# Kernel tuning notes

Measured on AMD Instinct MI355X. Metric: run time of the kernel, lower is better.

Reference implementation:

```python
import jax, jax.numpy as jnp
import numpy as np

H_MIN = -1.0
H_MAX = 1.0
B_SAT = 1.0
N = 256          # Preisach mesh size (n x n)
M = 4000         # number of applied-field time steps


def setup_inputs() -> dict:
    key = jax.random.key(0)
    k1, k2 = jax.random.split(key)
    # applied magnetic field history, spanning [h_min, h_max]
    h_data = jax.random.uniform(k1, (M,), dtype=jnp.float32, minval=-1.0, maxval=1.0)
    # raw (pre-softplus) hysteresis density vector, length n(n+1)/2
    raw = jax.random.normal(k2, (N * (N + 1) // 2,), dtype=jnp.float32)
    return {"h_data": h_data, "raw_hyst_density_vector": raw}


def reference(h_data, raw_hyst_density_vector):
    n = N
    dt = h_data.dtype
    x = jnp.linspace(0.0, 1.0, n, dtype=dt)
    # 'xy' indexing: xx varies along columns (beta thresholds), yy along rows (alpha thresholds)
    xx, yy = jnp.meshgrid(x, x)
    tril_mask = jnp.tril(jnp.ones((n, n), dtype=dt))

    # normalize_h
    h_norm = (h_data - H_MIN) / (H_MAX - H_MIN)
    hs = jnp.concatenate([jnp.full((1,), -H_MIN, dtype=dt), h_norm])  # (M+1,)
    # torch indexing hs[i-1] wraps to hs[-1] at i=0 -> roll by 1
    hp = jnp.roll(hs, 1)

    init = -jnp.ones((n, n), dtype=dt)

    def step(state, hh):
        h, p = hh
        swept_up = jnp.where(yy >= h, state, jnp.asarray(1.0, dt))    # sweep up: flip below alpha threshold
        swept_dn = jnp.where(xx <= h, state, jnp.asarray(-1.0, dt))   # sweep left: flip above beta threshold
        s = jnp.where(h > p, swept_up, jnp.where(h < p, swept_dn, state))
        s = s * tril_mask  # torch.tril each step
        return s, s

    _, states = jax.lax.scan(step, init, (hs, hp))  # (M+1, n, n)

    dens_vec = jax.nn.softplus(raw_hyst_density_vector)
    ti, tj = jnp.tril_indices(n)
    dens = jnp.zeros((n, n), dtype=dens_vec.dtype).at[ti, tj].set(dens_vec)
    a = B_SAT / jnp.sum(dens)

    # b[i] = sum(dens * states[i+1])
    b = jnp.einsum('tij,ij->t', states[1:], dens)
    return b * a
```

## Files before the change

### kernel.cpp

```cpp
#include <hip/hip_runtime.h>

#define NN 256
#define TT 32

__device__ __forceinline__ float softplus_f(float x) {
    if (x > 20.0f) return x;
    return log1pf(expf(x));
}

__global__ void __launch_bounds__(256)
kA(const float* __restrict__ h_g, const float* __restrict__ raw, int M, int G,
   float* __restrict__ PrefT, float* __restrict__ RowTot,
   int* __restrict__ steps_g, unsigned int* __restrict__ UDt)
{
    int b = blockIdx.x, tid = threadIdx.x;
    if (b < NN) {
        __shared__ float s[NN];
        float v = 0.0f;
        if (tid <= b) v = softplus_f(raw[b * (b + 1) / 2 + tid]);
        s[tid] = v;
        __syncthreads();
        for (int off = 1; off < NN; off <<= 1) {
            float add = (tid >= off) ? s[tid - off] : 0.0f;
            __syncthreads();
            s[tid] += add;
            __syncthreads();
        }
        PrefT[(tid + 1) * NN + b] = s[tid];
        if (tid == 0)      PrefT[b] = 0.0f;
        if (tid == NN - 1) RowTot[b] = s[tid];
    } else {
        __shared__ float xs[NN];
        __shared__ float hh[TT + 1];
        __shared__ int   dd[TT + 1];
        int c  = b - NN;
        int t0 = c * TT;
        int Tb = min(TT, M - t0);
        xs[tid] = (float)((double)tid / 255.0);
        __syncthreads();
        if (tid < Tb) {
            int tau = t0 + 1 + tid;
            float cur  = (h_g[tau - 1] + 1.0f) * 0.5f;
            float prev = (tau == 1) ? 1.0f : (h_g[tau - 2] + 1.0f) * 0.5f;
            int d = (cur > prev) ? 2 : ((cur < prev) ? 0 : 1);
            int lo = 0, hi = NN;
            while (lo < hi) { int m = (lo + hi) >> 1; if (xs[m] < cur) lo = m + 1; else hi = m; }
            int ih = lo;
            lo = 0; hi = NN;
            while (lo < hi) { int m = (lo + hi) >> 1; if (xs[m] <= cur) lo = m + 1; else hi = m; }
            int jh = lo;
            hh[1 + tid] = cur;
            dd[1 + tid] = d - 1;
            steps_g[tau] = d | (ih << 2) | (jh << 11);
        }
        __syncthreads();
        float xi = xs[tid];
        int Ue = 0, De = 0;
        for (int k = 1; k <= Tb; ++k) {
            float hv = hh[k]; int d = dd[k];
            if (d > 0 && hv > xi) Ue = t0 + k + 1;
            if (d < 0 && hv < xi) De = t0 + k + 1;
        }
        UDt[c * NN + tid] = (unsigned)Ue | ((unsigned)De << 16);
    }
}

__global__ void __launch_bounds__(256)
kB(const float* __restrict__ h_g, const int* __restrict__ steps_g,
   const unsigned int* __restrict__ UDt,
   const float* __restrict__ PrefT, const float* __restrict__ RowTot,
   float* __restrict__ out, int M)
{
    __shared__ int   rec_s[TT + 1];
    __shared__ int   Dv[NN];
    __shared__ float red[4 * (TT + 2)];
    __shared__ float tot[TT + 2];
    int b = blockIdx.x, tid = threadIdx.x;
    int t0 = b * TT;
    int Tb = min(TT, M - t0);

    if (tid < TT) rec_s[1 + tid] = (tid < Tb) ? steps_g[t0 + 1 + tid] : 0;
    float RT = RowTot[tid];

    float hsM = (h_g[M - 1] + 1.0f) * 0.5f;
    unsigned uM = (hsM < 1.0f && tid < NN - 1) ? 1u : 0u;
    unsigned dM = 0u;
    const unsigned int* p = UDt + tid;
    int k = 0;
    for (; k + 16 <= b; k += 16) {
        unsigned vv[16];
        #pragma unroll
        for (int u = 0; u < 16; ++u) vv[u] = p[(k + u) * NN];
        #pragma unroll
        for (int u = 0; u < 16; ++u) {
            unsigned ue = vv[u] & 0xFFFFu, de = vv[u] >> 16;
            if (ue > uM) uM = ue;
            if (de > dM) dM = de;
        }
    }
    for (; k < b; ++k) {
        unsigned v = p[k * NN];
        unsigned ue = v & 0xFFFFu, de = v >> 16;
        if (ue > uM) uM = ue;
        if (de > dM) dM = de;
    }
    int Ue = (int)uM;
    Dv[tid] = (int)dM;
    __syncthreads();

    float pk[TT + 1];
    #pragma unroll
    for (int kk = 1; kk <= TT; ++kk) {
        int jh = (rec_s[kk] >> 11) & 0x1FF;
        pk[kk] = PrefT[jh * NN + tid];
    }

    int lo = 0, hi = NN;
    while (lo < hi) { int m = (lo + hi) >> 1; if (Dv[m] < Ue) lo = m + 1; else hi = m; }
    int c = min(lo, tid + 1);
    float w = 2.0f * PrefT[c * NN + tid] - RT;

    float vals[TT + 2];
    vals[0] = RT; vals[1] = w;
    int cc = c; float ww = w;
    #pragma unroll
    for (int kk = 1; kk <= TT; ++kk) {
        float dl = 0.0f;
        if (kk <= Tb) {
            int rec = rec_s[kk];
            int d = rec & 3;
            if (d == 2) {
                int ih = (rec >> 2) & 0x1FF;
                if (tid < ih) { dl = RT - ww; ww = RT; cc = tid + 1; }
            } else if (d == 0) {
                int jh = (rec >> 11) & 0x1FF;
                if (cc > jh) { float wn = 2.0f * pk[kk] - RT; dl = wn - ww; ww = wn; cc = jh; }
            }
        }
        vals[1 + kk] = dl;
    }

    #pragma unroll
    for (int q = 0; q < TT + 2; ++q)
        for (int off = 32; off; off >>= 1)
            vals[q] += __shfl_down(vals[q], off, 64);
    int lane = tid & 63, wv = tid >> 6;
    if (lane == 0) {
        #pragma unroll
        for (int q = 0; q < TT + 2; ++q) red[wv * (TT + 2) + q] = vals[q];
    }
    __syncthreads();
    if (tid < TT + 2)
        tot[tid] = red[tid] + red[(TT + 2) + tid] + red[2 * (TT + 2) + tid] + red[3 * (TT + 2) + tid];
    __syncthreads();
    if (tid < TT) {
        float x = tot[2 + tid];
        #pragma unroll
        for (int off = 1; off < TT; off <<= 1) {
            float y = __shfl_up(x, off, 64);
            if (tid >= off) x += y;
        }
        if (tid < Tb) out[t0 + tid] = (tot[1] + x) * (1.0f / tot[0]);
    }
}

extern "C" void kernel_launch(void* const* d_in, const int* in_sizes, int n_in,
                              void* d_out, int out_size, void* d_ws, size_t ws_size,
                              hipStream_t stream) {
    const float* h   = (const float*)d_in[0];
    const float* raw = (const float*)d_in[1];
    float* out = (float*)d_out;
    int M = in_sizes[0];
    int G = (M + TT - 1) / TT;

    char* ws = (char*)d_ws;
    size_t off = 0;
    auto take = [&](size_t bytes) { size_t cur = off; off = (off + bytes + 255) & ~(size_t)255; return cur; };
    float*        PrefT  = (float*)(ws + take((size_t)(NN + 1) * NN * 4));
    float*        RowTot = (float*)(ws + take((size_t)NN * 4));
    int*          steps  = (int*)(ws + take((size_t)(M + 1) * 4));
    unsigned int* UDt    = (unsigned int*)(ws + take((size_t)G * NN * 4));

    kA<<<NN + G, 256, 0, stream>>>(h, raw, M, G, PrefT, RowTot, steps, UDt);
    kB<<<G, 256, 0, stream>>>(h, steps, UDt, PrefT, RowTot, out, M);
}
```

Before: 69.71 us.

## Fuse two-kernel Preisach pipeline into one kernel with per-block redundant recomputation

Merges the precompute kernel and the per-chunk evaluation kernel into a single launch. Each block rescans all prior time steps with atomicMax into shared buckets and suffix/prefix max scans, replacing the global UDt table. It also recomputes the softplus row prefix sums serially per thread, taking only the needed prefix values through a sorted request list in shared memory. This removes a launch and the global intermediates, but every block repeats O(M) step processing and O(N) softplus work per thread, about 125 blocks each doing redundant work.

```diff
diff --git a/kernel.cpp b/kernel.cpp
--- a/kernel.cpp
+++ b/kernel.cpp
@@ -9,120 +9,102 @@
 }
 
 __global__ void __launch_bounds__(256)
-kA(const float* __restrict__ h_g, const float* __restrict__ raw, int M, int G,
-   float* __restrict__ PrefT, float* __restrict__ RowTot,
-   int* __restrict__ steps_g, unsigned int* __restrict__ UDt)
+kFused(const float* __restrict__ h_g, const float* __restrict__ raw,
+       float* __restrict__ out, int M)
 {
-    int b = blockIdx.x, tid = threadIdx.x;
-    if (b < NN) {
-        __shared__ float s[NN];
-        float v = 0.0f;
-        if (tid <= b) v = softplus_f(raw[b * (b + 1) / 2 + tid]);
-        s[tid] = v;
-        __syncthreads();
-        for (int off = 1; off < NN; off <<= 1) {
-            float add = (tid >= off) ? s[tid - off] : 0.0f;
-            __syncthreads();
-            s[tid] += add;
-            __syncthreads();
-        }
-        PrefT[(tid + 1) * NN + b] = s[tid];
-        if (tid == 0)      PrefT[b] = 0.0f;
-        if (tid == NN - 1) RowTot[b] = s[tid];
-    } else {
-        __shared__ float xs[NN];
-        __shared__ float hh[TT + 1];
-        __shared__ int   dd[TT + 1];
-        int c  = b - NN;
-        int t0 = c * TT;
-        int Tb = min(TT, M - t0);
-        xs[tid] = (float)((double)tid / 255.0);
-        __syncthreads();
-        if (tid < Tb) {
-            int tau = t0 + 1 + tid;
-            float cur  = (h_g[tau - 1] + 1.0f) * 0.5f;
-            float prev = (tau == 1) ? 1.0f : (h_g[tau - 2] + 1.0f) * 0.5f;
-            int d = (cur > prev) ? 2 : ((cur < prev) ? 0 : 1);
-            int lo = 0, hi = NN;
-            while (lo < hi) { int m = (lo + hi) >> 1; if (xs[m] < cur) lo = m + 1; else hi = m; }
-            int ih = lo;
-            lo = 0; hi = NN;
-            while (lo < hi) { int m = (lo + hi) >> 1; if (xs[m] <= cur) lo = m + 1; else hi = m; }
-            int jh = lo;
-            hh[1 + tid] = cur;
-            dd[1 + tid] = d - 1;
-            steps_g[tau] = d | (ih << 2) | (jh << 11);
-        }
-        __syncthreads();
-        float xi = xs[tid];
-        int Ue = 0, De = 0;
-        for (int k = 1; k <= Tb; ++k) {
-            float hv = hh[k]; int d = dd[k];
-            if (d > 0 && hv > xi) Ue = t0 + k + 1;
-            if (d < 0 && hv < xi) De = t0 + k + 1;
-        }
-        UDt[c * NN + tid] = (unsigned)Ue | ((unsigned)De << 16);
-    }
-}
-
-__global__ void __launch_bounds__(256)
-kB(const float* __restrict__ h_g, const int* __restrict__ steps_g,
-   const unsigned int* __restrict__ UDt,
-   const float* __restrict__ PrefT, const float* __restrict__ RowTot,
-   float* __restrict__ out, int M)
-{
+    __shared__ float xs[NN];
+    __shared__ int   bestU[NN + 1];
+    __shared__ int   bestD[NN + 1];
     __shared__ int   rec_s[TT + 1];
-    __shared__ int   Dv[NN];
+    __shared__ int   plist[TT];
+    __shared__ float pk_s[TT][NN];
     __shared__ float red[4 * (TT + 2)];
     __shared__ float tot[TT + 2];
-    int b = blockIdx.x, tid = threadIdx.x;
-    int t0 = b * TT;
-    int Tb = min(TT, M - t0);
 
-    if (tid < TT) rec_s[1 + tid] = (tid < Tb) ? steps_g[t0 + 1 + tid] : 0;
-    float RT = RowTot[tid];
+    const int tid  = threadIdx.x;
+    const int c    = blockIdx.x;
+    const int t0   = c * TT;
+    const int Tb   = min(TT, M - t0);
+    const int tmax = t0 + Tb;
 
-    float hsM = (h_g[M - 1] + 1.0f) * 0.5f;
-    unsigned uM = (hsM < 1.0f && tid < NN - 1) ? 1u : 0u;
-    unsigned dM = 0u;
-    const unsigned int* p = UDt + tid;
-    int k = 0;
-    for (; k + 16 <= b; k += 16) {
-        unsigned vv[16];
-        #pragma unroll
-        for (int u = 0; u < 16; ++u) vv[u] = p[(k + u) * NN];
-        #pragma unroll
-        for (int u = 0; u < 16; ++u) {
-            unsigned ue = vv[u] & 0xFFFFu, de = vv[u] >> 16;
-            if (ue > uM) uM = ue;
-            if (de > dM) dM = de;
+    xs[tid] = (float)((double)tid / 255.0);
+    bestU[tid] = 0; bestD[tid] = 0;
+    if (tid == 0) { bestU[NN] = 0; bestD[NN] = 0; }
+    if (tid < TT) rec_s[1 + tid] = 0;
+    #pragma unroll
+    for (int kk = 0; kk < TT; ++kk) pk_s[kk][tid] = 0.0f;
+    __syncthreads();
+
+    for (int tau = 1 + tid; tau <= tmax; tau += NN) {
+        float cur  = (h_g[tau - 1] + 1.0f) * 0.5f;
+        float prev = (tau == 1) ? 1.0f : (h_g[tau - 2] + 1.0f) * 0.5f;
+        int d = (cur > prev) ? 2 : ((cur < prev) ? 0 : 1);
+        int g = (int)(cur * 255.0f) - 2;
+        int ih = max(g, 0);
+        while (ih < NN && xs[ih] < cur)  ++ih;
+        int jh = ih;
+        while (jh < NN && xs[jh] <= cur) ++jh;
+        if (tau <= t0) {
+            if (d == 2)      atomicMax(&bestU[ih], tau + 1);
+            else if (d == 0) atomicMax(&bestD[jh], tau + 1);
+        } else {
+            rec_s[tau - t0] = d | (ih << 2) | (jh << 11);
         }
     }
-    for (; k < b; ++k) {
-        unsigned v = p[k * NN];
-        unsigned ue = v & 0xFFFFu, de = v >> 16;
-        if (ue > uM) uM = ue;
-        if (de > dM) dM = de;
-    }
-    int Ue = (int)uM;
-    Dv[tid] = (int)dM;
     __syncthreads();
 
-    float pk[TT + 1];
-    #pragma unroll
-    for (int kk = 1; kk <= TT; ++kk) {
-        int jh = (rec_s[kk] >> 11) & 0x1FF;
-        pk[kk] = PrefT[jh * NN + tid];
+    for (int off = 1; off <= NN; off <<= 1) {
+        int vU = (tid + off <= NN) ? bestU[tid + off] : 0;
+        int vD = (tid >= off)      ? bestD[tid - off] : 0;
+        __syncthreads();
+        if (vU > bestU[tid]) bestU[tid] = vU;
+        if (vD > bestD[tid]) bestD[tid] = vD;
+        __syncthreads();
     }
+    int Ue = bestU[tid + 1];
+    float hsM = (h_g[M - 1] + 1.0f) * 0.5f;
+    if (hsM < 1.0f && tid < NN - 1) Ue = max(Ue, 1);
 
-    int lo = 0, hi = NN;
-    while (lo < hi) { int m = (lo + hi) >> 1; if (Dv[m] < Ue) lo = m + 1; else hi = m; }
-    int c = min(lo, tid + 1);
-    float w = 2.0f * PrefT[c * NN + tid] - RT;
+    {
+        int lo = 0, hi = NN;
+        while (lo < hi) { int m = (lo + hi) >> 1; if (bestD[m] < Ue) lo = m + 1; else hi = m; }
+        Ue = min(lo, tid + 1);
+    }
+    const int cc0 = Ue;
+
+    if (tid < TT) {
+        int jh_me = (rec_s[1 + tid] >> 11) & 0x1FF;
+        int rank = 0;
+        for (int j = 0; j < TT; ++j) {
+            int oj = (rec_s[1 + j] >> 11) & 0x1FF;
+            rank += (oj < jh_me) || (oj == jh_me && j < tid);
+        }
+        plist[rank] = (jh_me << 8) | tid;
+    }
+    __syncthreads();
+
+    const float* rowp = raw + (tid * (tid + 1)) / 2;
+    float s = 0.0f, pc0 = 0.0f;
+    {
+        int ptr = 0;
+        int nxt = plist[0];
+        while ((nxt >> 8) == 0) { ++ptr; nxt = (ptr < TT) ? plist[ptr] : 0x7FFFFFFF; }
+        for (int k = 0; k <= tid; ++k) {
+            s += softplus_f(rowp[k]);
+            if (k + 1 == cc0) pc0 = s;
+            while ((nxt >> 8) == k + 1) {
+                pk_s[nxt & 255][tid] = s;
+                ++ptr; nxt = (ptr < TT) ? plist[ptr] : 0x7FFFFFFF;
+            }
+        }
+    }
+    const float RT = s;
 
     float vals[TT + 2];
-    vals[0] = RT; vals[1] = w;
-    int cc = c; float ww = w;
+    vals[0] = RT;
+    float ww = 2.0f * pc0 - RT;
+    vals[1] = ww;
+    int cc = cc0;
     #pragma unroll
     for (int kk = 1; kk <= TT; ++kk) {
         float dl = 0.0f;
@@ -134,7 +116,7 @@
                 if (tid < ih) { dl = RT - ww; ww = RT; cc = tid + 1; }
             } else if (d == 0) {
                 int jh = (rec >> 11) & 0x1FF;
-                if (cc > jh) { float wn = 2.0f * pk[kk] - RT; dl = wn - ww; ww = wn; cc = jh; }
+                if (cc > jh) { float wn = 2.0f * pk_s[kk - 1][tid] - RT; dl = wn - ww; ww = wn; cc = jh; }
             }
         }
         vals[1 + kk] = dl;
@@ -172,15 +154,6 @@
     float* out = (float*)d_out;
     int M = in_sizes[0];
     int G = (M + TT - 1) / TT;
-
-    char* ws = (char*)d_ws;
-    size_t off = 0;
-    auto take = [&](size_t bytes) { size_t cur = off; off = (off + bytes + 255) & ~(size_t)255; return cur; };
-    float*        PrefT  = (float*)(ws + take((size_t)(NN + 1) * NN * 4));
-    float*        RowTot = (float*)(ws + take((size_t)NN * 4));
-    int*          steps  = (int*)(ws + take((size_t)(M + 1) * 4));
-    unsigned int* UDt    = (unsigned int*)(ws + take((size_t)G * NN * 4));
-
-    kA<<<NN + G, 256, 0, stream>>>(h, raw, M, G, PrefT, RowTot, steps, UDt);
-    kB<<<G, 256, 0, stream>>>(h, steps, UDt, PrefT, RowTot, out, M);
+    (void)d_ws; (void)ws_size; (void)n_in; (void)out_size;
+    kFused<<<G, NN, 0, stream>>>(h, raw, out, M);
 }
```

Result: slower. 199.0 us (+185.5%).

## Replace per-block max scans with exclusive prefix-max kernel, shrink chunk size, use wave-shuffle scan

Applied to the files above, without the earlier changes.

Each kB block used to re-scan every earlier chunk's UDt entries, which is quadratic work in the number of chunks. A new single-block kernel now computes an exclusive running max (PrefUD) once, and kB reads a single entry. The chunk size drops from 32 to 16, doubling the block count and shortening per-thread loops. The density prefix sum switches from a shared-memory Hillis-Steele scan to wave shuffles. This adds a serial one-block launch over G entries and an extra kernel launch.

```diff
diff --git a/kernel.cpp b/kernel.cpp
--- a/kernel.cpp
+++ b/kernel.cpp
@@ -1,7 +1,7 @@
 #include <hip/hip_runtime.h>
 
 #define NN 256
-#define TT 32
+#define TT 16
 
 __device__ __forceinline__ float softplus_f(float x) {
     if (x > 20.0f) return x;
@@ -15,20 +15,25 @@
 {
     int b = blockIdx.x, tid = threadIdx.x;
     if (b < NN) {
-        __shared__ float s[NN];
-        float v = 0.0f;
-        if (tid <= b) v = softplus_f(raw[b * (b + 1) / 2 + tid]);
-        s[tid] = v;
+        __shared__ float wsum[4];
+        float x = 0.0f;
+        if (tid <= b) x = softplus_f(raw[b * (b + 1) / 2 + tid]);
+        int lane = tid & 63, wv = tid >> 6;
+        #pragma unroll
+        for (int off = 1; off <= 32; off <<= 1) {
+            float y = __shfl_up(x, off, 64);
+            if (lane >= off) x += y;
+        }
+        if (lane == 63) wsum[wv] = x;
         __syncthreads();
-        for (int off = 1; off < NN; off <<= 1) {
-            float add = (tid >= off) ? s[tid - off] : 0.0f;
-            __syncthreads();
-            s[tid] += add;
-            __syncthreads();
-        }
-        PrefT[(tid + 1) * NN + b] = s[tid];
+        float add = 0.0f;
+        if (wv > 0) add += wsum[0];
+        if (wv > 1) add += wsum[1];
+        if (wv > 2) add += wsum[2];
+        x += add;
+        PrefT[(tid + 1) * NN + b] = x;
         if (tid == 0)      PrefT[b] = 0.0f;
-        if (tid == NN - 1) RowTot[b] = s[tid];
+        if (tid == NN - 1) RowTot[b] = x;
     } else {
         __shared__ float xs[NN];
         __shared__ float hh[TT + 1];
@@ -66,8 +71,39 @@
 }
 
 __global__ void __launch_bounds__(256)
-kB(const float* __restrict__ h_g, const int* __restrict__ steps_g,
-   const unsigned int* __restrict__ UDt,
+kM(const float* __restrict__ h_g, const unsigned int* __restrict__ UDt,
+   unsigned int* __restrict__ PrefUD, int M, int G)
+{
+    int tid = threadIdx.x;
+    float hsM = (h_g[M - 1] + 1.0f) * 0.5f;
+    unsigned u = (hsM < 1.0f && tid < NN - 1) ? 1u : 0u;
+    unsigned d = 0u;
+    const unsigned int* p = UDt + tid;
+    unsigned int* q = PrefUD + tid;
+    int k = 0;
+    for (; k + 8 <= G; k += 8) {
+        unsigned vv[8];
+        #pragma unroll
+        for (int uu = 0; uu < 8; ++uu) vv[uu] = p[(k + uu) * NN];
+        #pragma unroll
+        for (int uu = 0; uu < 8; ++uu) {
+            q[(k + uu) * NN] = u | (d << 16);
+            unsigned ue = vv[uu] & 0xFFFFu, de = vv[uu] >> 16;
+            if (ue > u) u = ue;
+            if (de > d) d = de;
+        }
+    }
+    for (; k < G; ++k) {
+        unsigned v = p[k * NN];
+        q[k * NN] = u | (d << 16);
+        unsigned ue = v & 0xFFFFu, de = v >> 16;
+        if (ue > u) u = ue;
+        if (de > d) d = de;
+    }
+}
+
+__global__ void __launch_bounds__(256)
+kB(const int* __restrict__ steps_g, const unsigned int* __restrict__ PrefUD,
    const float* __restrict__ PrefT, const float* __restrict__ RowTot,
    float* __restrict__ out, int M)
 {
@@ -82,30 +118,9 @@
     if (tid < TT) rec_s[1 + tid] = (tid < Tb) ? steps_g[t0 + 1 + tid] : 0;
     float RT = RowTot[tid];
 
-    float hsM = (h_g[M - 1] + 1.0f) * 0.5f;
-    unsigned uM = (hsM < 1.0f && tid < NN - 1) ? 1u : 0u;
-    unsigned dM = 0u;
-    const unsigned int* p = UDt + tid;
-    int k = 0;
-    for (; k + 16 <= b; k += 16) {
-        unsigned vv[16];
-        #pragma unroll
-        for (int u = 0; u < 16; ++u) vv[u] = p[(k + u) * NN];
-        #pragma unroll
-        for (int u = 0; u < 16; ++u) {
-            unsigned ue = vv[u] & 0xFFFFu, de = vv[u] >> 16;
-            if (ue > uM) uM = ue;
-            if (de > dM) dM = de;
-        }
-    }
-    for (; k < b; ++k) {
-        unsigned v = p[k * NN];
-        unsigned ue = v & 0xFFFFu, de = v >> 16;
-        if (ue > uM) uM = ue;
-        if (de > dM) dM = de;
-    }
-    int Ue = (int)uM;
-    Dv[tid] = (int)dM;
+    unsigned v = PrefUD[b * NN + tid];
+    int Ue = (int)(v & 0xFFFFu);
+    Dv[tid] = (int)(v >> 16);
     __syncthreads();
 
     float pk[TT + 1];
@@ -180,7 +195,9 @@
     float*        RowTot = (float*)(ws + take((size_t)NN * 4));
     int*          steps  = (int*)(ws + take((size_t)(M + 1) * 4));
     unsigned int* UDt    = (unsigned int*)(ws + take((size_t)G * NN * 4));
+    unsigned int* PrefUD = (unsigned int*)(ws + take((size_t)G * NN * 4));
 
     kA<<<NN + G, 256, 0, stream>>>(h, raw, M, G, PrefT, RowTot, steps, UDt);
-    kB<<<G, 256, 0, stream>>>(h, steps, UDt, PrefT, RowTot, out, M);
-}
+    kM<<<1, 256, 0, stream>>>(h, UDt, PrefUD, M, G);
+    kB<<<G, 256, 0, stream>>>(steps, PrefUD, PrefT, RowTot, out, M);
+}
```

Measured after the change: 77.20 us. 10.8% more time.
